# Kernel optimization log

Measured on AMD Instinct MI355X. Metric: run time of the kernel, lower is better.

## Reference

```python
import jax, jax.numpy as jnp
import numpy as np

NF, NC, LENGTH, BATCH = 64, 16, 2048, 256
WEIGHT_BI, WEIGHT_L2 = 0.01, 0.01
BETA = 2.5     # temporal soft-min/max sharpness (TemporalOperator beta=2.5)
KAPPA = 10.0   # logical soft-min/max sharpness (avm approximation)
EPSN = 1e-12


def setup_inputs() -> dict:
    key = jax.random.key(0)
    ks = jax.random.split(key, 11)
    x = jax.random.normal(ks[0], (BATCH, LENGTH, 2), dtype=jnp.float32)
    t1 = jax.random.uniform(ks[1], (NF,), minval=0.0, maxval=float(LENGTH // 2), dtype=jnp.float32)
    t2 = jax.random.uniform(ks[2], (NF,), minval=float(LENGTH // 2), maxval=float(LENGTH), dtype=jnp.float32)
    a = jax.random.uniform(ks[3], (NF,), dtype=jnp.float32)
    b = jax.random.uniform(ks[4], (NF,), dtype=jnp.float32)
    p1 = jax.random.uniform(ks[5], (NC, NF), dtype=jnp.float32)
    p2 = jax.random.uniform(ks[6], (1, NC), dtype=jnp.float32)
    tvar_temporal = jax.random.uniform(ks[7], (NF,), dtype=jnp.float32)
    tvar_logical1 = jax.random.uniform(ks[8], (NC,), dtype=jnp.float32)
    tvar_logical2 = jax.random.uniform(ks[9], (1,), dtype=jnp.float32)
    eps = jnp.full((1,), 0.1, dtype=jnp.float32)
    return dict(x=x, t1=t1, t2=t2, a=a, b=b, p1=p1, p2=p2,
                tvar_temporal=tvar_temporal, tvar_logical1=tvar_logical1,
                tvar_logical2=tvar_logical2, eps=eps)


def _ste(v, v_new):
    # torch clamps parameter .data under no_grad -> value changes, grad is identity
    return v + jax.lax.stop_gradient(v_new - v)


def _wsel(r, logw, sharp):
    # weighted soft-max (sharp>0) / soft-min (sharp<0) along last axis
    s = jax.nn.softmax(sharp * r + logw, axis=-1)
    return jnp.sum(s * r, axis=-1)


def reference(x, t1, t2, a, b, p1, p2, tvar_temporal, tvar_logical1, tvar_logical2, eps):
    # --- in-place parameter maintenance (clamp under no_grad in torch) ---
    p1 = _ste(p1, jnp.clip(p1, 0.0, 1.0))
    p2 = _ste(p2, jnp.clip(p2, 0.0, 1.0))
    tvt = _ste(tvar_temporal, jnp.clip(tvar_temporal, 0.0, 1.0))
    tvl1 = _ste(tvar_logical1, jnp.clip(tvar_logical1, 0.0, 1.0))
    tvl2 = _ste(tvar_logical2, jnp.clip(tvar_logical2, 0.0, 1.0))
    t1c = jnp.clip(t1, 0.0, LENGTH - 1.0)
    t2c = jnp.clip(t2, 0.0, LENGTH - 1.0)
    t1c = jnp.where(t1c >= t2c - 1.0, t2c - 1.0, t1c)
    t1u = _ste(t1, t1c)
    t2u = _ste(t2, t2c)

    # --- predicates (vectorized over all nf features; dim = i % 2) ---
    dims = jnp.arange(NF) % 2
    rp = a[None, None, :] * x[:, :, dims] - b[None, None, :]     # [B, T, NF]
    rp = jnp.transpose(rp, (0, 2, 1))                             # [B, NF, T]

    # --- temporal operators: smooth window [t1, t2] + soft min/max over time ---
    tg = jnp.arange(LENGTH, dtype=x.dtype)
    w = jax.nn.sigmoid(BETA * (tg[None, :] - t1u[:, None])) * \
        jax.nn.sigmoid(BETA * (t2u[:, None] - tg[None, :]))       # [NF, T]
    logw = jnp.log(w + EPSN)[None]                                # [1, NF, T]
    rmax = _wsel(rp, logw, BETA)                                  # eventually  [B, NF]
    rmin = _wsel(rp, logw, -BETA)                                 # always      [B, NF]
    r1 = tvt[None, :] * rmax + (1.0 - tvt[None, :]) * rmin        # [B, NF]

    # --- logical layer 1: weighted soft OR/AND over features, per clause ---
    logp1 = jnp.log(p1 + EPSN)[None]                              # [1, NC, NF]
    r1e = r1[:, None, :]                                          # [B, NC, NF]
    r_or = _wsel(r1e, logp1, KAPPA)
    r_and = _wsel(r1e, logp1, -KAPPA)
    r2 = tvl1[None, :] * r_or + (1.0 - tvl1[None, :]) * r_and     # [B, NC]

    # --- logical layer 2: combine clauses ---
    logp2 = jnp.log(p2[0] + EPSN)[None]                           # [1, NC]
    r_or2 = _wsel(r2, logp2, KAPPA)
    r_and2 = _wsel(r2, logp2, -KAPPA)
    r = tvl2[0] * r_or2 + (1.0 - tvl2[0]) * r_and2                # [B]

    # --- regularizers ---
    bi = WEIGHT_BI * (jnp.sum(tvt * (1.0 - tvt)) + jnp.sum(tvl1 * (1.0 - tvl1)) +
                      jnp.sum(tvl2 * (1.0 - tvl2)) + jnp.sum(p1 * (1.0 - p1)) +
                      jnp.sum(p2 * (1.0 - p2)))
    l2 = WEIGHT_L2 * (jnp.sum(p1 * p1) + jnp.sum(p2 * p2))
    reg = bi + l2
    return r, reg
```

## Files before the change

### kernel.cpp

```cpp
#include <hip/hip_runtime.h>
#include <math.h>

#define NF 64
#define NC 16
#define LEN 2048
#define BATCH 256
#define BETA 2.5f
#define KAPPA 10.0f
#define EPSN 1e-12f
#define LOG2E 1.4426950408889634f

#define TPB 1024
#define NQ (TPB / NF)
#define CHUNK (LEN / NQ)

__device__ __forceinline__ float clip01(float v) { return fminf(fmaxf(v, 0.0f), 1.0f); }

__device__ __forceinline__ float fexp2(float x) {
#if __has_builtin(__builtin_amdgcn_exp2f)
    return __builtin_amdgcn_exp2f(x);
#else
    return exp2f(x);
#endif
}

__device__ __forceinline__ float frcp(float x) {
#if __has_builtin(__builtin_amdgcn_rcpf)
    return __builtin_amdgcn_rcpf(x);
#else
    return 1.0f / x;
#endif
}

#define LW_BLOCKS ((NF * LEN / 4) / 256)

__global__ __launch_bounds__(256) void lw_reg_kernel(
    const float* __restrict__ t1, const float* __restrict__ t2,
    const float* __restrict__ p1, const float* __restrict__ p2,
    const float* __restrict__ tvt, const float* __restrict__ tvl1,
    const float* __restrict__ tvl2, float4* __restrict__ lwT4,
    float* __restrict__ out) {
    const int bid = blockIdx.x;
    const int tid = threadIdx.x;

    if (bid == LW_BLOCKS) {
        __shared__ float red[256];
        float acc = 0.0f;
        for (int i = tid; i < NC * NF; i += 256) {
            float p = clip01(p1[i]);
            acc += 0.01f * (p * (1.0f - p)) + 0.01f * (p * p);
        }
        if (tid < NC) {
            float p = clip01(p2[tid]);
            acc += 0.01f * (p * (1.0f - p)) + 0.01f * (p * p);
        }
        if (tid < NF) {
            float c = clip01(tvt[tid]);
            acc += 0.01f * (c * (1.0f - c));
        }
        if (tid < NC) {
            float c = clip01(tvl1[tid]);
            acc += 0.01f * (c * (1.0f - c));
        }
        if (tid == 0) {
            float c = clip01(tvl2[0]);
            acc += 0.01f * (c * (1.0f - c));
        }
        red[tid] = acc;
        __syncthreads();
        for (int s = 128; s > 0; s >>= 1) {
            if (tid < s) red[tid] += red[tid + s];
            __syncthreads();
        }
        if (tid == 0) out[BATCH] = red[0];
        return;
    }

    int idx = bid * 256 + tid;
    int f = idx & (NF - 1);
    int g = idx >> 6;
    float t1c = fminf(fmaxf(t1[f], 0.0f), (float)(LEN - 1));
    float t2c = fminf(fmaxf(t2[f], 0.0f), (float)(LEN - 1));
    t1c = fminf(t1c, t2c - 1.0f);
    float4 r;
#pragma unroll
    for (int j = 0; j < 4; ++j) {
        float t = (float)(4 * g + j);
        float su = 1.0f / (1.0f + __expf(-BETA * (t - t1c)));
        float sv = 1.0f / (1.0f + __expf(-BETA * (t2c - t)));
        ((float*)&r)[j] = __log2f(su * sv + EPSN);
    }
    lwT4[idx] = r;
}

__global__ __launch_bounds__(TPB) void fused_main(
    const float* __restrict__ x, const float4* __restrict__ lwT4,
    const float* __restrict__ av, const float* __restrict__ bv,
    const float* __restrict__ p1, const float* __restrict__ p2,
    const float* __restrict__ tvt_, const float* __restrict__ tvl1_,
    const float* __restrict__ tvl2_, float* __restrict__ out) {
    __shared__ float4 redQ[NQ][NF];
    __shared__ float r1s[NF];
    __shared__ float r2s[NC];

    const int b = blockIdx.x;
    const int tid = threadIdx.x;
    const int f = tid & (NF - 1);
    const int q = tid >> 6;
    const int ch = f & 1;

    const float B2 = BETA * LOG2E;
    const float KL = KAPPA * LOG2E;
    const float A2 = B2 * av[f];

    const int t0 = q * CHUNK;
    const float4* lw4 = lwT4 + (t0 >> 2) * NF + f;
    const float4* xp4 = (const float4*)(x + (size_t)b * (LEN * 2) + 2 * t0);

    float Sp0 = 0.f, Xp0 = 0.f, Sm0 = 0.f, Xm0 = 0.f;
    float Sp1 = 0.f, Xp1 = 0.f, Sm1 = 0.f, Xm1 = 0.f;
#pragma unroll 4
    for (int g = 0; g < CHUNK / 4; ++g) {
        float4 lw = lw4[g * NF];
        float4 u0 = xp4[2 * g];
        float4 u1 = xp4[2 * g + 1];
        float xa = ch ? u0.y : u0.x;
        float xb = ch ? u0.w : u0.z;
        float xc = ch ? u1.y : u1.x;
        float xd = ch ? u1.w : u1.z;
        float e;
        e = fexp2(fmaf(A2, xa, lw.x));  Sp0 += e; Xp0 = fmaf(e, xa, Xp0);
        e = fexp2(fmaf(-A2, xa, lw.x)); Sm0 += e; Xm0 = fmaf(e, xa, Xm0);
        e = fexp2(fmaf(A2, xb, lw.y));  Sp1 += e; Xp1 = fmaf(e, xb, Xp1);
        e = fexp2(fmaf(-A2, xb, lw.y)); Sm1 += e; Xm1 = fmaf(e, xb, Xm1);
        e = fexp2(fmaf(A2, xc, lw.z));  Sp0 += e; Xp0 = fmaf(e, xc, Xp0);
        e = fexp2(fmaf(-A2, xc, lw.z)); Sm0 += e; Xm0 = fmaf(e, xc, Xm0);
        e = fexp2(fmaf(A2, xd, lw.w));  Sp1 += e; Xp1 = fmaf(e, xd, Xp1);
        e = fexp2(fmaf(-A2, xd, lw.w)); Sm1 += e; Xm1 = fmaf(e, xd, Xm1);
    }

    redQ[q][f] = make_float4(Sp0 + Sp1, Xp0 + Xp1, Sm0 + Sm1, Xm0 + Xm1);
    __syncthreads();
    if (tid >= 64) return;

    const int l = tid;
    float ax = 0.f, ay = 0.f, az = 0.f, aw = 0.f;
#pragma unroll
    for (int s = 0; s < NQ; ++s) {
        float4 v = redQ[s][l];
        ax += v.x; ay += v.y; az += v.z; aw += v.w;
    }
    {
        float af = av[l], bf = bv[l];
        float tvt = clip01(tvt_[l]);
        float rmax = af * (ay / ax);
        float rmin = af * (aw / az);
        r1s[l] = tvt * rmax + (1.0f - tvt) * rmin - bf;
    }

    {
        const int c = l & 15;
        const int j = l >> 4;
        float so = 0.f, wo = 0.f, sa = 0.f, wa = 0.f;
#pragma unroll
        for (int i = 0; i < 16; ++i) {
            int ff = j * 16 + i;
            float r1v = r1s[ff];
            float lg = __log2f(clip01(p1[c * NF + ff]) + EPSN);
            float z = KL * r1v;
            float eo = fexp2(z + lg);
            float ea = fexp2(lg - z);
            so += eo; wo = fmaf(eo, r1v, wo);
            sa += ea; wa = fmaf(ea, r1v, wa);
        }
#pragma unroll
        for (int d = 16; d < 64; d <<= 1) {
            so += __shfl_xor(so, d);
            wo += __shfl_xor(wo, d);
            sa += __shfl_xor(sa, d);
            wa += __shfl_xor(wa, d);
        }
        if (l < NC) {
            float tvl1 = clip01(tvl1_[l]);
            r2s[l] = tvl1 * (wo / so) + (1.0f - tvl1) * (wa / sa);
        }
    }

    if (l == 0) {
        float so = 0.f, wo = 0.f, sa = 0.f, wa = 0.f;
#pragma unroll
        for (int c = 0; c < NC; ++c) {
            float lg = __log2f(clip01(p2[c]) + EPSN);
            float r2v = r2s[c];
            float z = KL * r2v;
            float eo = fexp2(z + lg);
            float ea = fexp2(lg - z);
            so += eo; wo = fmaf(eo, r2v, wo);
            sa += ea; wa = fmaf(ea, r2v, wa);
        }
        float tvl2 = clip01(tvl2_[0]);
        out[b] = tvl2 * (wo / so) + (1.0f - tvl2) * (wa / sa);
    }
}

__global__ __launch_bounds__(TPB) void fused_inline(
    const float* __restrict__ x, const float* __restrict__ t1g,
    const float* __restrict__ t2g, const float* __restrict__ av,
    const float* __restrict__ bv, const float* __restrict__ p1,
    const float* __restrict__ p2, const float* __restrict__ tvt_,
    const float* __restrict__ tvl1_, const float* __restrict__ tvl2_,
    float* __restrict__ out) {
    __shared__ float4 redQ[NQ][NF];
    __shared__ float r1s[NF];
    __shared__ float r2s[NC];

    const int b = blockIdx.x;
    const int tid = threadIdx.x;
    const int f = tid & (NF - 1);
    const int q = tid >> 6;
    const int ch = f & 1;

    const float B2 = BETA * LOG2E;
    const float KL = KAPPA * LOG2E;
    const float A2 = B2 * av[f];

    float t1c = fminf(fmaxf(t1g[f], 0.0f), (float)(LEN - 1));
    float t2c = fminf(fmaxf(t2g[f], 0.0f), (float)(LEN - 1));
    t1c = fminf(t1c, t2c - 1.0f);
    const float c1 = B2 * t1c;
    const float c2 = -B2 * t2c;

    const int t0 = q * CHUNK;
    const float4* xp4 = (const float4*)(x + (size_t)b * (LEN * 2) + 2 * t0);

    float Sp0 = 0.f, Xp0 = 0.f, Sm0 = 0.f, Xm0 = 0.f;
    float Sp1 = 0.f, Xp1 = 0.f, Sm1 = 0.f, Xm1 = 0.f;
#pragma unroll 4
    for (int k2 = 0; k2 < CHUNK / 2; ++k2) {
        float4 v = xp4[k2];
        float xa = ch ? v.y : v.x;
        float xb = ch ? v.w : v.z;
        float tfa = (float)(t0 + 2 * k2);
        float tfb = tfa + 1.0f;
        {
            float g1 = fmaf(-B2, tfa, c1);
            float g2 = fmaf(B2, tfa, c2);
            float den = (1.0f + fexp2(g1)) * (1.0f + fexp2(g2));
            float w = frcp(den);
            float P = fexp2(A2 * xa);
            float Pm = frcp(P);
            float tp = P * w, tm = Pm * w;
            Sp0 += tp; Xp0 = fmaf(tp, xa, Xp0);
            Sm0 += tm; Xm0 = fmaf(tm, xa, Xm0);
        }
        {
            float g1 = fmaf(-B2, tfb, c1);
            float g2 = fmaf(B2, tfb, c2);
            float den = (1.0f + fexp2(g1)) * (1.0f + fexp2(g2));
            float w = frcp(den);
            float P = fexp2(A2 * xb);
            float Pm = frcp(P);
            float tp = P * w, tm = Pm * w;
            Sp1 += tp; Xp1 = fmaf(tp, xb, Xp1);
            Sm1 += tm; Xm1 = fmaf(tm, xb, Xm1);
        }
    }

    redQ[q][f] = make_float4(Sp0 + Sp1, Xp0 + Xp1, Sm0 + Sm1, Xm0 + Xm1);

    if (b == 0 && q == NQ - 1) {
        const int l = f;
        float acc = 0.0f;
#pragma unroll
        for (int i = 0; i < 16; ++i) {
            float p = clip01(p1[i * NF + l]);
            acc += 0.01f * (p * (1.0f - p)) + 0.01f * (p * p);
        }
        {
            float c = clip01(tvt_[l]);
            acc += 0.01f * (c * (1.0f - c));
        }
        if (l < NC) {
            float p = clip01(p2[l]);
            acc += 0.01f * (p * (1.0f - p)) + 0.01f * (p * p);
            float c = clip01(tvl1_[l]);
            acc += 0.01f * (c * (1.0f - c));
        }
        if (l == 0) {
            float c = clip01(tvl2_[0]);
            acc += 0.01f * (c * (1.0f - c));
        }
#pragma unroll
        for (int d = 1; d < 64; d <<= 1) acc += __shfl_xor(acc, d);
        if (l == 0) out[BATCH] = acc;
    }

    __syncthreads();
    if (tid >= 64) return;

    const int l = tid;
    float ax = 0.f, ay = 0.f, az = 0.f, aw = 0.f;
#pragma unroll
    for (int s = 0; s < NQ; ++s) {
        float4 v = redQ[s][l];
        ax += v.x; ay += v.y; az += v.z; aw += v.w;
    }
    {
        float af = av[l], bf = bv[l];
        float tvt = clip01(tvt_[l]);
        float rmax = af * (ay / ax);
        float rmin = af * (aw / az);
        r1s[l] = tvt * rmax + (1.0f - tvt) * rmin - bf;
    }
    {
        const int c = l & 15;
        const int j = l >> 4;
        float so = 0.f, wo = 0.f, sa = 0.f, wa = 0.f;
#pragma unroll
        for (int i = 0; i < 16; ++i) {
            int ff = j * 16 + i;
            float r1v = r1s[ff];
            float lg = __log2f(clip01(p1[c * NF + ff]) + EPSN);
            float z = KL * r1v;
            float eo = fexp2(z + lg);
            float ea = fexp2(lg - z);
            so += eo; wo = fmaf(eo, r1v, wo);
            sa += ea; wa = fmaf(ea, r1v, wa);
        }
#pragma unroll
        for (int d = 16; d < 64; d <<= 1) {
            so += __shfl_xor(so, d);
            wo += __shfl_xor(wo, d);
            sa += __shfl_xor(sa, d);
            wa += __shfl_xor(wa, d);
        }
        if (l < NC) {
            float tvl1 = clip01(tvl1_[l]);
            r2s[l] = tvl1 * (wo / so) + (1.0f - tvl1) * (wa / sa);
        }
    }
    if (l == 0) {
        float so = 0.f, wo = 0.f, sa = 0.f, wa = 0.f;
#pragma unroll
        for (int c = 0; c < NC; ++c) {
            float lg = __log2f(clip01(p2[c]) + EPSN);
            float r2v = r2s[c];
            float z = KL * r2v;
            float eo = fexp2(z + lg);
            float ea = fexp2(lg - z);
            so += eo; wo = fmaf(eo, r2v, wo);
            sa += ea; wa = fmaf(ea, r2v, wa);
        }
        float tvl2 = clip01(tvl2_[0]);
        out[b] = tvl2 * (wo / so) + (1.0f - tvl2) * (wa / sa);
    }
}

extern "C" void kernel_launch(void* const* d_in, const int* in_sizes, int n_in,
                              void* d_out, int out_size, void* d_ws, size_t ws_size,
                              hipStream_t stream) {
    const float* x    = (const float*)d_in[0];
    const float* t1   = (const float*)d_in[1];
    const float* t2   = (const float*)d_in[2];
    const float* a    = (const float*)d_in[3];
    const float* bv   = (const float*)d_in[4];
    const float* p1   = (const float*)d_in[5];
    const float* p2   = (const float*)d_in[6];
    const float* tvt  = (const float*)d_in[7];
    const float* tvl1 = (const float*)d_in[8];
    const float* tvl2 = (const float*)d_in[9];
    float* out = (float*)d_out;

    const size_t lw_bytes = (size_t)(NF * LEN) * sizeof(float);

    if (d_ws && ws_size >= lw_bytes) {
        float4* lwT4 = (float4*)d_ws;
        lw_reg_kernel<<<LW_BLOCKS + 1, 256, 0, stream>>>(t1, t2, p1, p2, tvt, tvl1,
                                                         tvl2, lwT4, out);
        fused_main<<<BATCH, TPB, 0, stream>>>(x, lwT4, a, bv, p1, p2,
                                              tvt, tvl1, tvl2, out);
    } else {
        fused_inline<<<BATCH, TPB, 0, stream>>>(x, t1, t2, a, bv, p1, p2,
                                                tvt, tvl1, tvl2, out);
    }
}
```

Baseline: 26.05 us.

## Halve block size and pack exp-weighted accumulators into float2 vector ops

Cuts threads per block from 1024 to 512, so each thread handles twice as many timesteps and the shared reduction has fewer partial rows. The precomputed-weight kernel now keeps its sum and weighted-sum accumulators in 2-wide vectors, so the compiler can emit packed FMA instructions. The inline kernel merges its two accumulator sets into one, which shortens register use but lengthens the add dependency chain. Fewer threads per block lowers latency hiding per CU, in exchange for more work per thread and possibly packed math.

```diff
diff --git a/kernel.cpp b/kernel.cpp
--- a/kernel.cpp
+++ b/kernel.cpp
@@ -10,9 +10,11 @@
 #define EPSN 1e-12f
 #define LOG2E 1.4426950408889634f
 
-#define TPB 1024
+#define TPB 512
 #define NQ (TPB / NF)
 #define CHUNK (LEN / NQ)
+
+typedef float v2f __attribute__((ext_vector_type(2)));
 
 __device__ __forceinline__ float clip01(float v) { return fminf(fmaxf(v, 0.0f), 1.0f); }
 
@@ -21,14 +23,6 @@
     return __builtin_amdgcn_exp2f(x);
 #else
     return exp2f(x);
-#endif
-}
-
-__device__ __forceinline__ float frcp(float x) {
-#if __has_builtin(__builtin_amdgcn_rcpf)
-    return __builtin_amdgcn_rcpf(x);
-#else
-    return 1.0f / x;
 #endif
 }
 
@@ -112,13 +106,14 @@
     const float B2 = BETA * LOG2E;
     const float KL = KAPPA * LOG2E;
     const float A2 = B2 * av[f];
+    const v2f Apm = {A2, -A2};
 
     const int t0 = q * CHUNK;
     const float4* lw4 = lwT4 + (t0 >> 2) * NF + f;
     const float4* xp4 = (const float4*)(x + (size_t)b * (LEN * 2) + 2 * t0);
 
-    float Sp0 = 0.f, Xp0 = 0.f, Sm0 = 0.f, Xm0 = 0.f;
-    float Sp1 = 0.f, Xp1 = 0.f, Sm1 = 0.f, Xm1 = 0.f;
+    v2f SXp0 = {0.f, 0.f}, SXm0 = {0.f, 0.f};
+    v2f SXp1 = {0.f, 0.f}, SXm1 = {0.f, 0.f};
 #pragma unroll 4
     for (int g = 0; g < CHUNK / 4; ++g) {
         float4 lw = lw4[g * NF];
@@ -128,18 +123,43 @@
         float xb = ch ? u0.w : u0.z;
         float xc = ch ? u1.y : u1.x;
         float xd = ch ? u1.w : u1.z;
-        float e;
-        e = fexp2(fmaf(A2, xa, lw.x));  Sp0 += e; Xp0 = fmaf(e, xa, Xp0);
-        e = fexp2(fmaf(-A2, xa, lw.x)); Sm0 += e; Xm0 = fmaf(e, xa, Xm0);
-        e = fexp2(fmaf(A2, xb, lw.y));  Sp1 += e; Xp1 = fmaf(e, xb, Xp1);
-        e = fexp2(fmaf(-A2, xb, lw.y)); Sm1 += e; Xm1 = fmaf(e, xb, Xm1);
-        e = fexp2(fmaf(A2, xc, lw.z));  Sp0 += e; Xp0 = fmaf(e, xc, Xp0);
-        e = fexp2(fmaf(-A2, xc, lw.z)); Sm0 += e; Xm0 = fmaf(e, xc, Xm0);
-        e = fexp2(fmaf(A2, xd, lw.w));  Sp1 += e; Xp1 = fmaf(e, xd, Xp1);
-        e = fexp2(fmaf(-A2, xd, lw.w)); Sm1 += e; Xm1 = fmaf(e, xd, Xm1);
-    }
-
-    redQ[q][f] = make_float4(Sp0 + Sp1, Xp0 + Xp1, Sm0 + Sm1, Xm0 + Xm1);
+        {
+            v2f z = Apm * xa + (v2f){lw.x, lw.x};
+            v2f e0 = {fexp2(z.x), fexp2(z.x)};
+            v2f e1 = {fexp2(z.y), fexp2(z.y)};
+            v2f m = {1.0f, xa};
+            SXp0 += e0 * m;
+            SXm0 += e1 * m;
+        }
+        {
+            v2f z = Apm * xb + (v2f){lw.y, lw.y};
+            v2f e0 = {fexp2(z.x), fexp2(z.x)};
+            v2f e1 = {fexp2(z.y), fexp2(z.y)};
+            v2f m = {1.0f, xb};
+            SXp1 += e0 * m;
+            SXm1 += e1 * m;
+        }
+        {
+            v2f z = Apm * xc + (v2f){lw.z, lw.z};
+            v2f e0 = {fexp2(z.x), fexp2(z.x)};
+            v2f e1 = {fexp2(z.y), fexp2(z.y)};
+            v2f m = {1.0f, xc};
+            SXp0 += e0 * m;
+            SXm0 += e1 * m;
+        }
+        {
+            v2f z = Apm * xd + (v2f){lw.w, lw.w};
+            v2f e0 = {fexp2(z.x), fexp2(z.x)};
+            v2f e1 = {fexp2(z.y), fexp2(z.y)};
+            v2f m = {1.0f, xd};
+            SXp1 += e0 * m;
+            SXm1 += e1 * m;
+        }
+    }
+    v2f SXp = SXp0 + SXp1;
+    v2f SXm = SXm0 + SXm1;
+
+    redQ[q][f] = make_float4(SXp.x, SXp.y, SXm.x, SXm.y);
     __syncthreads();
     if (tid >= 64) return;
 
@@ -201,6 +221,14 @@
         float tvl2 = clip01(tvl2_[0]);
         out[b] = tvl2 * (wo / so) + (1.0f - tvl2) * (wa / sa);
     }
+}
+
+__device__ __forceinline__ float frcp(float x) {
+#if __has_builtin(__builtin_amdgcn_rcpf)
+    return __builtin_amdgcn_rcpf(x);
+#else
+    return 1.0f / x;
+#endif
 }
 
 __global__ __launch_bounds__(TPB) void fused_inline(
@@ -233,8 +261,7 @@
     const int t0 = q * CHUNK;
     const float4* xp4 = (const float4*)(x + (size_t)b * (LEN * 2) + 2 * t0);
 
-    float Sp0 = 0.f, Xp0 = 0.f, Sm0 = 0.f, Xm0 = 0.f;
-    float Sp1 = 0.f, Xp1 = 0.f, Sm1 = 0.f, Xm1 = 0.f;
+    float Sp = 0.f, Xp = 0.f, Sm = 0.f, Xm = 0.f;
 #pragma unroll 4
     for (int k2 = 0; k2 < CHUNK / 2; ++k2) {
         float4 v = xp4[k2];
@@ -250,8 +277,8 @@
             float P = fexp2(A2 * xa);
             float Pm = frcp(P);
             float tp = P * w, tm = Pm * w;
-            Sp0 += tp; Xp0 = fmaf(tp, xa, Xp0);
-            Sm0 += tm; Xm0 = fmaf(tm, xa, Xm0);
+            Sp += tp; Xp = fmaf(tp, xa, Xp);
+            Sm += tm; Xm = fmaf(tm, xa, Xm);
         }
         {
             float g1 = fmaf(-B2, tfb, c1);
@@ -261,12 +288,12 @@
             float P = fexp2(A2 * xb);
             float Pm = frcp(P);
             float tp = P * w, tm = Pm * w;
-            Sp1 += tp; Xp1 = fmaf(tp, xb, Xp1);
-            Sm1 += tm; Xm1 = fmaf(tm, xb, Xm1);
-        }
-    }
-
-    redQ[q][f] = make_float4(Sp0 + Sp1, Xp0 + Xp1, Sm0 + Sm1, Xm0 + Xm1);
+            Sp += tp; Xp = fmaf(tp, xb, Xp);
+            Sm += tm; Xm = fmaf(tm, xb, Xm);
+        }
+    }
+
+    redQ[q][f] = make_float4(Sp, Xp, Sm, Xm);
 
     if (b == 0 && q == NQ - 1) {
         const int l = f;
```

After: 26.95 us. +3.5%, slower.
